# Kernel optimization log

Hardware: AMD Instinct MI355X
Metric: run time of the kernel (lower is better)

The kernel has to match this reference:

```python
import jax, jax.numpy as jnp
import numpy as np


def setup_inputs() -> dict:
    key = jax.random.key(0)
    k1, k2 = jax.random.split(key)
    shape = (16, 3, 512, 512)
    y_true = jax.random.uniform(k1, shape, dtype=jnp.float32)
    y_pred = jax.random.uniform(k2, shape, dtype=jnp.float32)
    return {"y_true": y_true, "y_pred": y_pred}


def reference(y_true, y_pred):
    B, C, W, H = y_true.shape
    percent = 0.4
    index = int(W * H * percent - 1)  # quantile index into ascending sort
    # gray1 = mean over the 3 channels of y_pred  -> [B, W, H]
    gray = (y_pred[:, 0] + y_pred[:, 1] + y_pred[:, 2]) / 3.0
    # torch.topk(-gray, n)[0][:, index] == -(ascending-sorted gray)[index]
    thr = jnp.sort(gray.reshape(B, W * H), axis=1)[:, index]  # [B]
    mask = (gray <= thr[:, None, None]).astype(y_pred.dtype)  # [B, W, H]
    mask = mask[:, None, :, :]  # broadcast over 3 channels
    # mask*|y_pred - y_true| == |mask*y_pred - mask*y_true| since mask in {0,1}
    d = jnp.abs(y_pred - y_true)
    w = mask * 0.8 + (1.0 - mask) * 0.2
    return jnp.mean(w * d)
```

## Files before the change

### kernel.cpp

```cpp
#include <hip/hip_runtime.h>
#include <stdint.h>

#define NB 16
#define NPIX 262144
#define K_RANK 104856u
#define NB1 4096
#define NSEG 16
#define SEGCAP 16384
#define PAD(i) ((i) + ((i) >> 4))

__device__ inline void scan4096(const unsigned* __restrict__ sh, unsigned* wave_sums,
                                int tid, unsigned r,
                                unsigned* out_digit, unsigned* out_res) {
    unsigned sum = 0;
    #pragma unroll
    for (int j = 0; j < 16; ++j) sum += sh[tid * 17 + j];
    unsigned inc = sum;
    for (int off = 1; off < 64; off <<= 1) {
        unsigned v = __shfl_up(inc, off);
        if ((tid & 63) >= off) inc += v;
    }
    if ((tid & 63) == 63) wave_sums[tid >> 6] = inc;
    __syncthreads();
    unsigned woff = 0;
    for (int w = 0; w < (tid >> 6); ++w) woff += wave_sums[w];
    const unsigned excl = woff + inc - sum;
    if (r >= excl && r < excl + sum) {
        unsigned cum = excl;
        unsigned d   = (unsigned)(tid * 16);
        #pragma unroll
        for (int j = 0; j < 16; ++j) {
            unsigned c = sh[tid * 17 + j];
            if (cum + c > r) { d = (unsigned)(tid * 16 + j); break; }
            cum += c;
        }
        *out_digit = d;
        *out_res   = r - cum;
    }
}

__global__ void k_hist(const float* __restrict__ yp, unsigned* __restrict__ hist1,
                       unsigned* __restrict__ zr, int zcount) {
    __shared__ unsigned h[NB1];
    const int tid = threadIdx.x;
    const int gtid = blockIdx.x * 256 + tid;
    if (gtid < zcount) zr[gtid] = 0;
    for (int i = tid; i < NB1; i += 256) h[i] = 0;
    __syncthreads();

    const int blk   = blockIdx.x;
    const int b     = blk >> 8;
    const int chunk = blk & 255;
    const long base = (long)b * 3 * NPIX;
    const int  o    = (chunk * 256 + tid) * 4;

    const float4 c0 = *(const float4*)(yp + base + o);
    const float4 c1 = *(const float4*)(yp + base + NPIX + o);
    const float4 c2 = *(const float4*)(yp + base + 2 * NPIX + o);

    atomicAdd(&h[__float_as_uint((c0.x + c1.x + c2.x) / 3.0f) >> 20], 1u);
    atomicAdd(&h[__float_as_uint((c0.y + c1.y + c2.y) / 3.0f) >> 20], 1u);
    atomicAdd(&h[__float_as_uint((c0.z + c1.z + c2.z) / 3.0f) >> 20], 1u);
    atomicAdd(&h[__float_as_uint((c0.w + c1.w + c2.w) / 3.0f) >> 20], 1u);
    __syncthreads();

    unsigned* gh = hist1 + b * NB1;
    for (int i = tid; i < NB1; i += 256) {
        unsigned v = h[i];
        if (v) atomicAdd(&gh[i], v);
    }
}

__global__ void k_scan(const unsigned* __restrict__ hist1,
                       unsigned* __restrict__ selbin, unsigned* __restrict__ resrank) {
    __shared__ unsigned sh[NB1 + (NB1 >> 4)];
    __shared__ unsigned wave_sums[4];
    const int b   = blockIdx.x;
    const int tid = threadIdx.x;
    const unsigned* hb = hist1 + b * NB1;
    for (int i = tid; i < NB1; i += 256) sh[PAD(i)] = hb[i];
    __syncthreads();
    scan4096(sh, wave_sums, tid, K_RANK, &selbin[b], &resrank[b]);
}

__global__ void k_main(const float* __restrict__ yp, const float* __restrict__ yt,
                       const unsigned* __restrict__ selbin, unsigned* __restrict__ ccnt,
                       uint2* __restrict__ cand, double* __restrict__ accum) {
    __shared__ uint2 buf[1024];
    __shared__ unsigned cnt, s_base;
    __shared__ float wsum[4];
    const int tid   = threadIdx.x;
    const int blk   = blockIdx.x;
    const int b     = blk >> 8;
    const int chunk = blk & 255;
    const int seg   = chunk >> 4;
    if (tid == 0) cnt = 0;

    const long base = (long)b * 3 * NPIX;
    const int  o    = (chunk * 256 + tid) * 4;

    const float4 p0 = *(const float4*)(yp + base + o);
    const float4 p1 = *(const float4*)(yp + base + NPIX + o);
    const float4 p2 = *(const float4*)(yp + base + 2 * NPIX + o);
    const float4 t0 = *(const float4*)(yt + base + o);
    const float4 t1 = *(const float4*)(yt + base + NPIX + o);
    const float4 t2 = *(const float4*)(yt + base + 2 * NPIX + o);
    const unsigned sel = selbin[b];
    __syncthreads();

    float s = 0.0f;
    {
        float g = (p0.x + p1.x + p2.x) / 3.0f;
        unsigned u = __float_as_uint(g);
        float d = fabsf(p0.x - t0.x) + fabsf(p1.x - t1.x) + fabsf(p2.x - t2.x);
        unsigned bin = u >> 20;
        s += ((bin < sel) ? 0.8f : 0.2f) * d;
        if (bin == sel) { unsigned i = atomicAdd(&cnt, 1u); buf[i] = make_uint2(u, __float_as_uint(d)); }
    }
    {
        float g = (p0.y + p1.y + p2.y) / 3.0f;
        unsigned u = __float_as_uint(g);
        float d = fabsf(p0.y - t0.y) + fabsf(p1.y - t1.y) + fabsf(p2.y - t2.y);
        unsigned bin = u >> 20;
        s += ((bin < sel) ? 0.8f : 0.2f) * d;
        if (bin == sel) { unsigned i = atomicAdd(&cnt, 1u); buf[i] = make_uint2(u, __float_as_uint(d)); }
    }
    {
        float g = (p0.z + p1.z + p2.z) / 3.0f;
        unsigned u = __float_as_uint(g);
        float d = fabsf(p0.z - t0.z) + fabsf(p1.z - t1.z) + fabsf(p2.z - t2.z);
        unsigned bin = u >> 20;
        s += ((bin < sel) ? 0.8f : 0.2f) * d;
        if (bin == sel) { unsigned i = atomicAdd(&cnt, 1u); buf[i] = make_uint2(u, __float_as_uint(d)); }
    }
    {
        float g = (p0.w + p1.w + p2.w) / 3.0f;
        unsigned u = __float_as_uint(g);
        float d = fabsf(p0.w - t0.w) + fabsf(p1.w - t1.w) + fabsf(p2.w - t2.w);
        unsigned bin = u >> 20;
        s += ((bin < sel) ? 0.8f : 0.2f) * d;
        if (bin == sel) { unsigned i = atomicAdd(&cnt, 1u); buf[i] = make_uint2(u, __float_as_uint(d)); }
    }
    __syncthreads();

    if (tid == 0) s_base = cnt ? atomicAdd(&ccnt[b * NSEG + seg], cnt) : 0u;
    __syncthreads();
    const unsigned nn = cnt;
    const unsigned bs = s_base;
    uint2* dst = cand + ((long)b * NSEG + seg) * SEGCAP;
    for (unsigned i = (unsigned)tid; i < nn; i += 256) {
        unsigned slot = bs + i;
        if (slot < SEGCAP) dst[slot] = buf[i];
    }

    for (int off = 32; off > 0; off >>= 1) s += __shfl_down(s, off);
    if ((tid & 63) == 0) wsum[tid >> 6] = s;
    __syncthreads();
    if (tid == 0) {
        float tot = wsum[0] + wsum[1] + wsum[2] + wsum[3];
        atomicAdd(&accum[(blk & 63) * 16], (double)tot);
    }
}

__global__ void k_sel(const uint2* __restrict__ cand, const unsigned* __restrict__ resrank,
                      const unsigned* __restrict__ ccnt, double* __restrict__ accum) {
    __shared__ unsigned sh[NB1 + (NB1 >> 4)];
    __shared__ float    sd[NB1 + (NB1 >> 4)];
    __shared__ unsigned h3[256];
    __shared__ float    sd3[256];
    __shared__ unsigned wave_sums[4];
    __shared__ unsigned s_bin2, s_r3, s_low;
    __shared__ float red[4];
    const int tid = threadIdx.x;
    const int b   = blockIdx.x;

    if (tid == 0) { s_bin2 = 0; s_r3 = 0; s_low = 0; }
    const unsigned r2 = resrank[b];

    for (int i = tid; i < NB1; i += 256) { sh[PAD(i)] = 0u; sd[PAD(i)] = 0.0f; }
    h3[tid] = 0u; sd3[tid] = 0.0f;
    __syncthreads();

    for (int seg = 0; seg < NSEG; ++seg) {
        const unsigned n = min(ccnt[b * NSEG + seg], (unsigned)SEGCAP);
        const uint2* cb = cand + ((long)b * NSEG + seg) * SEGCAP;
        for (unsigned base0 = 0; base0 < n; base0 += 1024) {
            const unsigned idx = base0 + (unsigned)tid * 4u;
            if (idx + 4 <= n) {
                const uint4 a = *(const uint4*)(cb + idx);
                const uint4 c = *(const uint4*)(cb + idx + 2);
                unsigned bn;
                bn = (a.x >> 8) & 0xFFFu; atomicAdd(&sh[PAD(bn)], 1u); atomicAdd(&sd[PAD(bn)], __uint_as_float(a.y));
                bn = (a.z >> 8) & 0xFFFu; atomicAdd(&sh[PAD(bn)], 1u); atomicAdd(&sd[PAD(bn)], __uint_as_float(a.w));
                bn = (c.x >> 8) & 0xFFFu; atomicAdd(&sh[PAD(bn)], 1u); atomicAdd(&sd[PAD(bn)], __uint_as_float(c.y));
                bn = (c.z >> 8) & 0xFFFu; atomicAdd(&sh[PAD(bn)], 1u); atomicAdd(&sd[PAD(bn)], __uint_as_float(c.w));
            } else {
                for (unsigned k = idx; k < n && k < idx + 4u; ++k) {
                    uint2 v = cb[k];
                    unsigned bn = (v.x >> 8) & 0xFFFu;
                    atomicAdd(&sh[PAD(bn)], 1u); atomicAdd(&sd[PAD(bn)], __uint_as_float(v.y));
                }
            }
        }
    }
    __syncthreads();

    scan4096(sh, wave_sums, tid, r2, &s_bin2, &s_r3);
    __syncthreads();
    const unsigned bin2 = s_bin2;
    const unsigned r3   = s_r3;

    float lp = 0.0f;
    #pragma unroll
    for (int j = 0; j < 16; ++j) {
        unsigned gb = (unsigned)(tid * 16 + j);
        if (gb < bin2) lp += sd[tid * 17 + j];
    }
    for (int off = 32; off > 0; off >>= 1) lp += __shfl_down(lp, off);
    if ((tid & 63) == 0) red[tid >> 6] = lp;
    __syncthreads();
    const float S_pre = red[0] + red[1] + red[2] + red[3];
    __syncthreads();

    for (int seg = 0; seg < NSEG; ++seg) {
        const unsigned n = min(ccnt[b * NSEG + seg], (unsigned)SEGCAP);
        const uint2* cb = cand + ((long)b * NSEG + seg) * SEGCAP;
        for (unsigned base0 = 0; base0 < n; base0 += 1024) {
            const unsigned idx = base0 + (unsigned)tid * 4u;
            if (idx + 4 <= n) {
                const uint4 a = *(const uint4*)(cb + idx);
                const uint4 c = *(const uint4*)(cb + idx + 2);
                if (((a.x >> 8) & 0xFFFu) == bin2) { atomicAdd(&h3[a.x & 0xFFu], 1u); atomicAdd(&sd3[a.x & 0xFFu], __uint_as_float(a.y)); }
                if (((a.z >> 8) & 0xFFFu) == bin2) { atomicAdd(&h3[a.z & 0xFFu], 1u); atomicAdd(&sd3[a.z & 0xFFu], __uint_as_float(a.w)); }
                if (((c.x >> 8) & 0xFFFu) == bin2) { atomicAdd(&h3[c.x & 0xFFu], 1u); atomicAdd(&sd3[c.x & 0xFFu], __uint_as_float(c.y)); }
                if (((c.z >> 8) & 0xFFFu) == bin2) { atomicAdd(&h3[c.z & 0xFFu], 1u); atomicAdd(&sd3[c.z & 0xFFu], __uint_as_float(c.w)); }
            } else {
                for (unsigned k = idx; k < n && k < idx + 4u; ++k) {
                    uint2 v = cb[k];
                    if (((v.x >> 8) & 0xFFFu) == bin2) { atomicAdd(&h3[v.x & 0xFFu], 1u); atomicAdd(&sd3[v.x & 0xFFu], __uint_as_float(v.y)); }
                }
            }
        }
    }
    __syncthreads();

    const unsigned sum = h3[tid];
    unsigned inc = sum;
    for (int off = 1; off < 64; off <<= 1) {
        unsigned v = __shfl_up(inc, off);
        if ((tid & 63) >= off) inc += v;
    }
    if ((tid & 63) == 63) wave_sums[tid >> 6] = inc;
    __syncthreads();
    unsigned woff = 0;
    for (int w = 0; w < (tid >> 6); ++w) woff += wave_sums[w];
    const unsigned excl = woff + inc - sum;
    if (sum > 0 && r3 >= excl && r3 < excl + sum) s_low = (unsigned)tid;
    __syncthreads();
    const unsigned low = s_low;

    float l2 = ((unsigned)tid <= low) ? sd3[tid] : 0.0f;
    for (int off = 32; off > 0; off >>= 1) l2 += __shfl_down(l2, off);
    if ((tid & 63) == 0) red[tid >> 6] = l2;
    __syncthreads();
    if (tid == 0) {
        float S_b2 = red[0] + red[1] + red[2] + red[3];
        atomicAdd(&accum[(b & 63) * 16], 0.6 * ((double)S_pre + (double)S_b2));
    }
}

__global__ void k_final(const double* __restrict__ accum, float* __restrict__ out) {
    const int tid = threadIdx.x;
    double v = accum[tid * 16];
    for (int off = 32; off > 0; off >>= 1) v += __shfl_down(v, off);
    if (tid == 0) out[0] = (float)(v / 12582912.0);
}

extern "C" void kernel_launch(void* const* d_in, const int* in_sizes, int n_in,
                              void* d_out, int out_size, void* d_ws, size_t ws_size,
                              hipStream_t stream) {
    const float* yt = (const float*)d_in[0];
    const float* yp = (const float*)d_in[1];
    float* out = (float*)d_out;
    char* ws = (char*)d_ws;

    unsigned* hist1  = (unsigned*)(ws);
    double*   accum  = (double*)(ws + 262144);
    unsigned* ccnt   = (unsigned*)(ws + 270336);
    unsigned* zr     = (unsigned*)(ws + 262144);
    unsigned* selbin = (unsigned*)(ws + 271360);
    unsigned* resrnk = (unsigned*)(ws + 271424);
    uint2*    cand   = (uint2*)(ws + (1 << 20));
    const int zcount = (8192 + 1024) / 4;

    hipMemsetAsync(hist1, 0, 262144, stream);

    k_hist <<<4096, 256, 0, stream>>>(yp, hist1, zr, zcount);
    k_scan <<<NB,   256, 0, stream>>>(hist1, selbin, resrnk);
    k_main <<<4096, 256, 0, stream>>>(yp, yt, selbin, ccnt, cand, accum);
    k_sel  <<<NB,   256, 0, stream>>>(cand, resrnk, ccnt, accum);
    k_final<<<1,    64,  0, stream>>>(accum, out);
}
```

Before: 181.2 us.

## Stage candidates in LDS and drop per-bin float sum histogram in k_sel

The selection kernel now copies candidate entries into a shared-memory staging buffer during the first histogram pass. The second pass, which computes the prefix sum and the fine histogram, reads from LDS instead of re-reading global memory. The float sum histogram and its atomics are removed, and the below-threshold sum is accumulated directly in the second pass. Loads are now per-wave per-segment scalar uint2 reads instead of vectorized uint4, which may reduce load efficiency. Candidates that overflow the staging buffer fall back to global reads.

```diff
diff --git a/kernel.cpp b/kernel.cpp
--- a/kernel.cpp
+++ b/kernel.cpp
@@ -7,6 +7,7 @@
 #define NB1 4096
 #define NSEG 16
 #define SEGCAP 16384
+#define STAGE_CAP 12288
 #define PAD(i) ((i) + ((i) >> 4))
 
 __device__ inline void scan4096(const unsigned* __restrict__ sh, unsigned* wave_sums,
@@ -165,40 +166,46 @@
 __global__ void k_sel(const uint2* __restrict__ cand, const unsigned* __restrict__ resrank,
                       const unsigned* __restrict__ ccnt, double* __restrict__ accum) {
     __shared__ unsigned sh[NB1 + (NB1 >> 4)];
-    __shared__ float    sd[NB1 + (NB1 >> 4)];
+    __shared__ uint2    stage[STAGE_CAP];
     __shared__ unsigned h3[256];
     __shared__ float    sd3[256];
     __shared__ unsigned wave_sums[4];
+    __shared__ unsigned segn[NSEG], sego[NSEG + 1];
     __shared__ unsigned s_bin2, s_r3, s_low;
     __shared__ float red[4];
-    const int tid = threadIdx.x;
-    const int b   = blockIdx.x;
+    const int tid  = threadIdx.x;
+    const int b    = blockIdx.x;
+    const int wave = tid >> 6;
+    const int lane = tid & 63;
 
     if (tid == 0) { s_bin2 = 0; s_r3 = 0; s_low = 0; }
+    if (tid < NSEG) segn[tid] = min(ccnt[b * NSEG + tid], (unsigned)SEGCAP);
     const unsigned r2 = resrank[b];
-
-    for (int i = tid; i < NB1; i += 256) { sh[PAD(i)] = 0u; sd[PAD(i)] = 0.0f; }
+    for (int i = tid; i < NB1; i += 256) sh[PAD(i)] = 0u;
     h3[tid] = 0u; sd3[tid] = 0.0f;
     __syncthreads();
-
-    for (int seg = 0; seg < NSEG; ++seg) {
-        const unsigned n = min(ccnt[b * NSEG + seg], (unsigned)SEGCAP);
-        const uint2* cb = cand + ((long)b * NSEG + seg) * SEGCAP;
-        for (unsigned base0 = 0; base0 < n; base0 += 1024) {
-            const unsigned idx = base0 + (unsigned)tid * 4u;
-            if (idx + 4 <= n) {
-                const uint4 a = *(const uint4*)(cb + idx);
-                const uint4 c = *(const uint4*)(cb + idx + 2);
-                unsigned bn;
-                bn = (a.x >> 8) & 0xFFFu; atomicAdd(&sh[PAD(bn)], 1u); atomicAdd(&sd[PAD(bn)], __uint_as_float(a.y));
-                bn = (a.z >> 8) & 0xFFFu; atomicAdd(&sh[PAD(bn)], 1u); atomicAdd(&sd[PAD(bn)], __uint_as_float(a.w));
-                bn = (c.x >> 8) & 0xFFFu; atomicAdd(&sh[PAD(bn)], 1u); atomicAdd(&sd[PAD(bn)], __uint_as_float(c.y));
-                bn = (c.z >> 8) & 0xFFFu; atomicAdd(&sh[PAD(bn)], 1u); atomicAdd(&sd[PAD(bn)], __uint_as_float(c.w));
-            } else {
-                for (unsigned k = idx; k < n && k < idx + 4u; ++k) {
-                    uint2 v = cb[k];
-                    unsigned bn = (v.x >> 8) & 0xFFFu;
-                    atomicAdd(&sh[PAD(bn)], 1u); atomicAdd(&sd[PAD(bn)], __uint_as_float(v.y));
+    if (tid == 0) {
+        unsigned acc = 0;
+        #pragma unroll
+        for (int s2 = 0; s2 < NSEG; ++s2) { sego[s2] = acc; acc += segn[s2]; }
+        sego[NSEG] = acc;
+    }
+    __syncthreads();
+    const unsigned T = sego[NSEG];
+    const uint2* cb = cand + (long)b * NSEG * SEGCAP;
+
+    for (int s = wave; s < NSEG; s += 4) {
+        const unsigned n  = segn[s];
+        const unsigned o0 = sego[s];
+        const uint2* p = cb + (long)s * SEGCAP;
+        for (unsigned i = (unsigned)lane * 4u; i < n; i += 256u) {
+            #pragma unroll
+            for (unsigned k = 0; k < 4; ++k) {
+                if (i + k < n) {
+                    uint2 v = p[i + k];
+                    atomicAdd(&sh[PAD((v.x >> 8) & 0xFFFu)], 1u);
+                    unsigned pos = o0 + i + k;
+                    if (pos < STAGE_CAP) stage[pos] = v;
                 }
             }
         }
@@ -211,38 +218,31 @@
     const unsigned r3   = s_r3;
 
     float lp = 0.0f;
-    #pragma unroll
-    for (int j = 0; j < 16; ++j) {
-        unsigned gb = (unsigned)(tid * 16 + j);
-        if (gb < bin2) lp += sd[tid * 17 + j];
-    }
-    for (int off = 32; off > 0; off >>= 1) lp += __shfl_down(lp, off);
-    if ((tid & 63) == 0) red[tid >> 6] = lp;
-    __syncthreads();
-    const float S_pre = red[0] + red[1] + red[2] + red[3];
-    __syncthreads();
-
-    for (int seg = 0; seg < NSEG; ++seg) {
-        const unsigned n = min(ccnt[b * NSEG + seg], (unsigned)SEGCAP);
-        const uint2* cb = cand + ((long)b * NSEG + seg) * SEGCAP;
-        for (unsigned base0 = 0; base0 < n; base0 += 1024) {
-            const unsigned idx = base0 + (unsigned)tid * 4u;
-            if (idx + 4 <= n) {
-                const uint4 a = *(const uint4*)(cb + idx);
-                const uint4 c = *(const uint4*)(cb + idx + 2);
-                if (((a.x >> 8) & 0xFFFu) == bin2) { atomicAdd(&h3[a.x & 0xFFu], 1u); atomicAdd(&sd3[a.x & 0xFFu], __uint_as_float(a.y)); }
-                if (((a.z >> 8) & 0xFFFu) == bin2) { atomicAdd(&h3[a.z & 0xFFu], 1u); atomicAdd(&sd3[a.z & 0xFFu], __uint_as_float(a.w)); }
-                if (((c.x >> 8) & 0xFFFu) == bin2) { atomicAdd(&h3[c.x & 0xFFu], 1u); atomicAdd(&sd3[c.x & 0xFFu], __uint_as_float(c.y)); }
-                if (((c.z >> 8) & 0xFFFu) == bin2) { atomicAdd(&h3[c.z & 0xFFu], 1u); atomicAdd(&sd3[c.z & 0xFFu], __uint_as_float(c.w)); }
-            } else {
-                for (unsigned k = idx; k < n && k < idx + 4u; ++k) {
-                    uint2 v = cb[k];
-                    if (((v.x >> 8) & 0xFFFu) == bin2) { atomicAdd(&h3[v.x & 0xFFu], 1u); atomicAdd(&sd3[v.x & 0xFFu], __uint_as_float(v.y)); }
+    const unsigned Ts = (T < (unsigned)STAGE_CAP) ? T : (unsigned)STAGE_CAP;
+    for (unsigned i = (unsigned)tid; i < Ts; i += 256u) {
+        uint2 v = stage[i];
+        unsigned bn = (v.x >> 8) & 0xFFFu;
+        if (bn < bin2) lp += __uint_as_float(v.y);
+        else if (bn == bin2) { atomicAdd(&h3[v.x & 0xFFu], 1u); atomicAdd(&sd3[v.x & 0xFFu], __uint_as_float(v.y)); }
+    }
+    if (T > (unsigned)STAGE_CAP) {
+        for (int s = wave; s < NSEG; s += 4) {
+            const unsigned n = segn[s], o0 = sego[s];
+            const uint2* p = cb + (long)s * SEGCAP;
+            for (unsigned i = (unsigned)lane; i < n; i += 64u) {
+                if (o0 + i >= (unsigned)STAGE_CAP) {
+                    uint2 v = p[i];
+                    unsigned bn = (v.x >> 8) & 0xFFFu;
+                    if (bn < bin2) lp += __uint_as_float(v.y);
+                    else if (bn == bin2) { atomicAdd(&h3[v.x & 0xFFu], 1u); atomicAdd(&sd3[v.x & 0xFFu], __uint_as_float(v.y)); }
                 }
             }
         }
     }
-    __syncthreads();
+    for (int off = 32; off > 0; off >>= 1) lp += __shfl_down(lp, off);
+    if (lane == 0) red[wave] = lp;
+    __syncthreads();
+    const float S_pre = red[0] + red[1] + red[2] + red[3];
 
     const unsigned sum = h3[tid];
     unsigned inc = sum;
```

Result: faster. 168.0 us (-7.3%).
